# Kernel tuning notes

Hardware: AMD Instinct MI355X
Metric: run time of the kernel (lower is better)

The kernel has to match this reference:

```python
import jax, jax.numpy as jnp
import numpy as np

OUT = (4, 4, 4)       # output_size
SCALE = 1.0           # spatial_scale


def _axis_masks(start, length, n_bins, dim):
    """PyTorch AdaptiveMaxPool bin membership along one axis.

    bin i covers global indices [start + floor(i*L/O), start + ceil((i+1)*L/O)).
    Returns bool mask of shape [N, n_bins, dim].
    """
    i = jnp.arange(n_bins)
    bs = start[:, None] + (i[None, :] * length[:, None]) // n_bins
    be = start[:, None] - ((-(i[None, :] + 1) * length[:, None]) // n_bins)  # ceil div
    p = jnp.arange(dim)
    return (p[None, None, :] >= bs[:, :, None]) & (p[None, None, :] < be[:, :, None])


def _roi_pool_3d(x, rois):
    feat = x[0]                     # [C, X, Y, Z]
    C, X, Y, Z = feat.shape
    # rois: [1, N, 7] = (batch_idx, x0, y0, z0, x1, y1, z1); scale + round as in torch code
    r = jnp.round(rois[0, :, 1:].astype(jnp.float32) * SCALE).astype(jnp.int32)  # [N, 6]
    starts = r[:, :3]               # [N, 3]
    lens = r[:, 3:] + 1 - starts    # inclusive ends -> lengths, >= 1
    O1, O2, O3 = OUT
    mx = _axis_masks(starts[:, 0], lens[:, 0], O1, X)   # [N, O1, X]
    my = _axis_masks(starts[:, 1], lens[:, 1], O2, Y)   # [N, O2, Y]
    mz = _axis_masks(starts[:, 2], lens[:, 2], O3, Z)   # [N, O3, Z]
    neg = jnp.finfo(feat.dtype).min
    # separable max-reductions: z, then y, then x (loops are over the tiny fixed bin counts)
    t = jnp.stack([jnp.max(jnp.where(mz[:, k][:, None, None, None, :], feat[None], neg), axis=-1)
                   for k in range(O3)], axis=-1)                      # [N, C, X, Y, O3]
    t = jnp.stack([jnp.max(jnp.where(my[:, j][:, None, None, :, None], t, neg), axis=3)
                   for j in range(O2)], axis=3)                       # [N, C, X, O2, O3]
    t = jnp.stack([jnp.max(jnp.where(mx[:, i][:, None, :, None, None], t, neg), axis=2)
                   for i in range(O1)], axis=2)                       # [N, C, O1, O2, O3]
    return t


def setup_inputs() -> dict:
    key = jax.random.key(0)
    C, D, N = 64, 48, 16
    x = jax.random.normal(key, (1, C, D, D, D), dtype=jnp.float32)
    rng = np.random.default_rng(0)
    lens = rng.integers(8, 25, size=(N, 3))                       # roi extents in [8, 24]
    starts = np.array([rng.integers(0, D - L + 1) for L in lens.reshape(-1)]).reshape(N, 3)
    ends = starts + lens - 1                                      # inclusive ends, < D
    rois = np.concatenate([np.zeros((N, 1), np.int32),
                           starts.astype(np.int32),
                           ends.astype(np.int32)], axis=1)        # [N, 7]
    return {"input": x, "rois": jnp.asarray(rois[None], dtype=jnp.int32)}


def reference(input, rois):
    return _roi_pool_3d(input, rois)   # [N, C, 4, 4, 4]
```

## Files before the change

kernel.cpp:

```cpp
#include <hip/hip_runtime.h>
#include <float.h>

#define NC 64
#define DIM 48
#define NROI 16

__global__ __launch_bounds__(256) void roipool3d_kernel(
    const float* __restrict__ feat,
    const int*   __restrict__ rois,
    float*       __restrict__ out)
{
    int t = threadIdx.x;
    int bin = t >> 2;
    int p   = t & 3;
    int c = blockIdx.x & (NC - 1);
    int n = blockIdx.x >> 6;

    int k = bin & 3;
    int j = (bin >> 2) & 3;
    int i = bin >> 4;

    const int* r = rois + n * 7;
    int sx = r[1], sy = r[2], sz = r[3];
    int lx = r[4] + 1 - sx;
    int ly = r[5] + 1 - sy;
    int lz = r[6] + 1 - sz;

    int bx0 = sx + ((i * lx) >> 2);
    int bx1 = sx + (((i + 1) * lx + 3) >> 2);
    int by0 = sy + ((j * ly) >> 2);
    int by1 = sy + (((j + 1) * ly + 3) >> 2);
    int bz0 = sz + ((k * lz) >> 2);
    int bz1 = sz + (((k + 1) * lz + 3) >> 2);

    int nx = bx1 - bx0;
    int ny = by1 - by0;
    int nrows = nx * ny;

    const float* base = feat + (size_t)c * (DIM * DIM * DIM);

    float m0 = -FLT_MAX, m1 = -FLT_MAX;
    for (int rr = p; rr < nrows; rr += 4) {
        int x = bx0 + rr / ny;
        int y = by0 + rr % ny;
        const float* row = base + x * (DIM * DIM) + y * DIM;
        int z = bz0;
        for (; z + 1 < bz1; z += 2) {
            m0 = fmaxf(m0, row[z]);
            m1 = fmaxf(m1, row[z + 1]);
        }
        if (z < bz1) m0 = fmaxf(m0, row[z]);
    }
    float m = fmaxf(m0, m1);

    m = fmaxf(m, __shfl_xor(m, 1));
    m = fmaxf(m, __shfl_xor(m, 2));

    if (p == 0) out[(blockIdx.x << 6) + bin] = m;
}

extern "C" void kernel_launch(void* const* d_in, const int* in_sizes, int n_in,
                              void* d_out, int out_size, void* d_ws, size_t ws_size,
                              hipStream_t stream) {
    const float* feat = (const float*)d_in[0];
    const int*   rois = (const int*)d_in[1];
    float*       out  = (float*)d_out;

    roipool3d_kernel<<<dim3(NROI * NC), dim3(256), 0, stream>>>(feat, rois, out);
}
```

Before: 75.63 us.

## Stage ROI box in LDS with coalesced loads before per-bin max reduction

```diff
diff --git a/kernel.cpp b/kernel.cpp
--- a/kernel.cpp
+++ b/kernel.cpp
@@ -4,52 +4,65 @@
 #define NC 64
 #define DIM 48
 #define NROI 16
+#define MAXL 24
+#define LDS_FLOATS (MAXL * MAXL * (MAXL + 1))
 
 __global__ __launch_bounds__(256) void roipool3d_kernel(
     const float* __restrict__ feat,
     const int*   __restrict__ rois,
     float*       __restrict__ out)
 {
+    __shared__ float box[LDS_FLOATS];
+
     int t = threadIdx.x;
-    int bin = t >> 2;
-    int p   = t & 3;
     int c = blockIdx.x & (NC - 1);
     int n = blockIdx.x >> 6;
-
-    int k = bin & 3;
-    int j = (bin >> 2) & 3;
-    int i = bin >> 4;
 
     const int* r = rois + n * 7;
     int sx = r[1], sy = r[2], sz = r[3];
     int lx = r[4] + 1 - sx;
     int ly = r[5] + 1 - sy;
     int lz = r[6] + 1 - sz;
+    int lzp = lz + 1;
 
-    int bx0 = sx + ((i * lx) >> 2);
-    int bx1 = sx + (((i + 1) * lx + 3) >> 2);
-    int by0 = sy + ((j * ly) >> 2);
-    int by1 = sy + (((j + 1) * ly + 3) >> 2);
-    int bz0 = sz + ((k * lz) >> 2);
-    int bz1 = sz + (((k + 1) * lz + 3) >> 2);
+    const float* base = feat + (size_t)c * (DIM * DIM * DIM)
+                      + sx * (DIM * DIM) + sy * DIM + sz;
 
-    int nx = bx1 - bx0;
-    int ny = by1 - by0;
-    int nrows = nx * ny;
+    {
+        int zt = t & 31;
+        int rw = t >> 5;
+        int nrows = lx * ly;
+        if (zt < lz) {
+            int x = 0, y = rw;
+            for (int rr = rw; rr < nrows; rr += 8) {
+                box[rr * lzp + zt] = base[x * (DIM * DIM) + y * DIM + zt];
+                y += 8;
+                if (y >= ly) { y -= ly; ++x; }
+            }
+        }
+    }
+    __syncthreads();
 
-    const float* base = feat + (size_t)c * (DIM * DIM * DIM);
+    int bin = t >> 2;
+    int p   = t & 3;
+    int k = bin & 3;
+    int j = (bin >> 2) & 3;
+    int i = bin >> 4;
+
+    int bx0 = (i * lx) >> 2,  bx1 = ((i + 1) * lx + 3) >> 2;
+    int by0 = (j * ly) >> 2,  by1 = ((j + 1) * ly + 3) >> 2;
+    int bz0 = (k * lz) >> 2,  bz1 = ((k + 1) * lz + 3) >> 2;
 
     float m0 = -FLT_MAX, m1 = -FLT_MAX;
-    for (int rr = p; rr < nrows; rr += 4) {
-        int x = bx0 + rr / ny;
-        int y = by0 + rr % ny;
-        const float* row = base + x * (DIM * DIM) + y * DIM;
-        int z = bz0;
-        for (; z + 1 < bz1; z += 2) {
-            m0 = fmaxf(m0, row[z]);
-            m1 = fmaxf(m1, row[z + 1]);
+    int z0 = bz0 + p;
+    int z1 = z0 + 4;
+    for (int x = bx0; x < bx1; ++x) {
+        int rowx = x * ly;
+        for (int y = by0; y < by1; ++y) {
+            int rowa = (rowx + y) * lzp;
+            if (z0 < bz1) m0 = fmaxf(m0, box[rowa + z0]);
+            if (z1 < bz1) m1 = fmaxf(m1, box[rowa + z1]);
         }
-        if (z < bz1) m0 = fmaxf(m0, row[z]);
     }
     float m = fmaxf(m0, m1);
 
```

Result: slower. 92.12 us (+21.8%).
